# Optimization experiments

Measured on AMD Instinct MI355X. Metric: run time of the kernel, lower is better.

## Reference

```python
import jax, jax.numpy as jnp
import numpy as np

S, B, T, D = 256, 32, 24, 512


def setup_inputs() -> dict:
    key = jax.random.key(0)
    ks = jax.random.split(key, 30)
    def lin(k, out_d, in_d):
        kw, kb = jax.random.split(k)
        w = jax.random.normal(kw, (out_d, in_d), jnp.float32) * 0.02
        b = jax.random.normal(kb, (out_d,), jnp.float32) * 0.02
        return w, b
    inp = {
        'context_output': jax.random.normal(ks[0], (S, B, D), jnp.float32),
        'context_hidden_state': jax.random.normal(ks[1], (B, D), jnp.float32),
        'question_output': jax.random.normal(ks[2], (T, B, D), jnp.float32),
        'question_hidden_state': jax.random.normal(ks[3], (B, D), jnp.float32),
        'image_output': jax.random.normal(ks[4], (S, B, D), jnp.float32),
        'image_hidden_state': jax.random.normal(ks[5], (B, D), jnp.float32),
    }
    inp['fc1_w'], inp['fc1_b'] = lin(ks[6], D, D)
    inp['fc2_w'], inp['fc2_b'] = lin(ks[7], D, D)
    inp['dm_w'], inp['dm_b'] = lin(ks[8], D, D)
    inp['ms_w'], inp['ms_b'] = lin(ks[9], 1, D)
    inp['rm_w'], inp['rm_b'] = lin(ks[10], D, D)
    inp['qm_w'], inp['qm_b'] = lin(ks[11], D, D)
    inp['rr_w'], inp['rr_b'] = lin(ks[12], D, D)
    inp['rg_w'], inp['rg_b'] = lin(ks[13], D, D)
    inp['qg_w'], inp['qg_b'] = lin(ks[14], D, D)
    return inp


def reference(context_output, context_hidden_state, question_output,
              question_hidden_state, image_output, image_hidden_state,
              fc1_w, fc1_b, fc2_w, fc2_b, dm_w, dm_b, ms_w, ms_b,
              rm_w, rm_b, qm_w, qm_b, rr_w, rr_b, rg_w, rg_b, qg_w, qg_b):
    # context_output/image_output: [S,B,D] -> co: [B,S,D]
    co = (jnp.einsum('sbd,ed->bse', context_output, fc1_w) + fc1_b
          + jnp.einsum('sbd,ed->bse', image_output, fc2_w) + fc2_b)
    # linear_dm(co) is loop-invariant; compute once (same math as original)
    co_dm = jnp.einsum('bsd,ed->bse', co, dm_w) + dm_b  # [B,S,D]

    def step(r, q):
        # r: [B,D] (the original's [B,1,D] memory), q: [B,D]
        add = (r @ rm_w.T + rm_b) + (q @ qm_w.T + qm_b)  # [B,D]
        m = jnp.tanh(co_dm + add[:, None, :])             # [B,S,D]
        logits = m @ ms_w.T + ms_b                        # [B,S,1]
        s = jax.nn.softmax(logits, axis=1)                # softmax over S
        r_new = jnp.sum(s * co, axis=1) + jnp.tanh(r @ rr_w.T + rr_b)
        return r_new, None

    r0 = jnp.zeros((B, D), co.dtype)
    r, _ = jax.lax.scan(step, r0, question_output)  # scan over T steps
    g = (r @ rg_w.T + rg_b) + (question_hidden_state @ qg_w.T + qg_b)
    return g
```

## Files before the change

### kernel.cpp

```cpp
#include <hip/hip_runtime.h>

#define S_DIM 256
#define B_DIM 32
#define T_DIM 24
#define D_DIM 512

typedef short short8 __attribute__((ext_vector_type(8)));
typedef unsigned short ushort8 __attribute__((ext_vector_type(8)));
typedef float float4v __attribute__((ext_vector_type(4)));
typedef unsigned long long u64;

#define ATOM_ST64(p, v) __hip_atomic_store((p), (v), __ATOMIC_RELAXED, __HIP_MEMORY_SCOPE_AGENT)
#define ATOM_LD64(p)    __hip_atomic_load((p), __ATOMIC_RELAXED, __HIP_MEMORY_SCOPE_AGENT)

__device__ __forceinline__ float bf2f(unsigned short u) {
  union { unsigned int i; float f; } v; v.i = ((unsigned int)u) << 16; return v.f;
}
__device__ __forceinline__ unsigned short f2bf(float f) {
  union { float f; unsigned int i; } v; v.f = f;
  unsigned int i = v.i;
  return (unsigned short)((i + 0x7fffu + ((i >> 16) & 1u)) >> 16);
}
__device__ __forceinline__ float tanh_fast(float x) {
  float p = __builtin_amdgcn_exp2f(x * 2.885390082f);
  return 1.f - 2.f * __builtin_amdgcn_rcpf(1.f + p);
}
__device__ __forceinline__ void gload_lds16(const void* g, void* l) {
  __builtin_amdgcn_global_load_lds(
      (const __attribute__((address_space(1))) void*)g,
      (__attribute__((address_space(3))) void*)l, 16, 0, 0);
}
__device__ __forceinline__ u64 pack_tag(unsigned tag, float v) {
  union { float f; unsigned u; } c; c.f = v;
  return ((u64)tag << 32) | (u64)c.u;
}
__device__ __forceinline__ float unpack_val(u64 v) {
  union { unsigned u; float f; } c; c.u = (unsigned)v; return c.f;
}
__device__ __forceinline__ float poll_val(const u64* p, unsigned tag) {
  u64 v = ATOM_LD64(p);
  while ((unsigned)(v >> 32) != tag) { __builtin_amdgcn_s_sleep(1); v = ATOM_LD64(p); }
  return unpack_val(v);
}

template<bool A_F32, bool W_F32, bool DUAL, bool PERMUTE>
__global__ __launch_bounds__(256)
void gemm_nt(const void* __restrict__ A1v, const void* __restrict__ A2v,
             const void* __restrict__ W1v, const void* __restrict__ W2v,
             const float* __restrict__ bias1,
             const float* __restrict__ bias2,
             unsigned short* __restrict__ out)
{
  __shared__ unsigned short At[128 * 32] __attribute__((aligned(16)));
  __shared__ unsigned short Bt[128 * 32] __attribute__((aligned(16)));

  const int tid  = threadIdx.x;
  const int wid  = tid >> 6;
  const int lane = tid & 63;
  const int bm = blockIdx.x, bn = blockIdx.y;
  const int wm = (wid & 1) * 64, wn = (wid >> 1) * 64;

  float4v acc[4][4];
#pragma unroll
  for (int i = 0; i < 4; ++i)
#pragma unroll
    for (int jj = 0; jj < 4; ++jj) acc[i][jj] = (float4v){0.f, 0.f, 0.f, 0.f};

  const int NK = DUAL ? 32 : 16;
  for (int it = 0; it < NK; ++it) {
    const int kk = it * 32;
    const void* Av = A1v;
    const void* Wv = W1v;
    int ks = kk;
    if (DUAL && kk >= 512) { Av = A2v; Wv = W2v; ks = kk - 512; }

    __syncthreads();
    if (A_F32) {
      const float* Af = (const float*)Av;
      const int r = tid >> 1, h = tid & 1;
      const float4v* p = (const float4v*)(Af + (size_t)(bm * 128 + r) * 512 + ks + h * 16);
      float4v x0 = p[0], x1 = p[1], x2 = p[2], x3 = p[3];
      ushort8 u0, u1;
#pragma unroll
      for (int i = 0; i < 4; ++i) {
        u0[i] = f2bf(x0[i]); u0[i + 4] = f2bf(x1[i]);
        u1[i] = f2bf(x2[i]); u1[i + 4] = f2bf(x3[i]);
      }
      *(ushort8*)&At[r * 32 + h * 16] = u0;
      *(ushort8*)&At[r * 32 + h * 16 + 8] = u1;
    } else {
      const unsigned short* Ab = (const unsigned short*)Av;
#pragma unroll
      for (int i = 0; i < 2; ++i)
        gload_lds16(Ab + (size_t)(bm * 128 + wid * 32 + i * 16 + (lane >> 2)) * 512 + ks + (lane & 3) * 8,
                    &At[(wid * 32 + i * 16) * 32]);
    }
    if (W_F32) {
      const float* Wf = (const float*)Wv;
      const int r = tid >> 1, h = tid & 1;
      const float4v* p = (const float4v*)(Wf + (size_t)(bn * 128 + r) * 512 + ks + h * 16);
      float4v x0 = p[0], x1 = p[1], x2 = p[2], x3 = p[3];
      ushort8 u0, u1;
#pragma unroll
      for (int i = 0; i < 4; ++i) {
        u0[i] = f2bf(x0[i]); u0[i + 4] = f2bf(x1[i]);
        u1[i] = f2bf(x2[i]); u1[i + 4] = f2bf(x3[i]);
      }
      *(ushort8*)&Bt[r * 32 + h * 16] = u0;
      *(ushort8*)&Bt[r * 32 + h * 16 + 8] = u1;
    } else {
      const unsigned short* Wb = (const unsigned short*)Wv;
#pragma unroll
      for (int i = 0; i < 2; ++i)
        gload_lds16(Wb + (size_t)(bn * 128 + wid * 32 + i * 16 + (lane >> 2)) * 512 + ks + (lane & 3) * 8,
                    &Bt[(wid * 32 + i * 16) * 32]);
    }
    __syncthreads();

    short8 fa[4], fb[4];
#pragma unroll
    for (int mi = 0; mi < 4; ++mi)
      fa[mi] = *(const short8*)&At[(wm + mi * 16 + (lane & 15)) * 32 + (lane >> 4) * 8];
#pragma unroll
    for (int ni = 0; ni < 4; ++ni)
      fb[ni] = *(const short8*)&Bt[(wn + ni * 16 + (lane & 15)) * 32 + (lane >> 4) * 8];
#pragma unroll
    for (int mi = 0; mi < 4; ++mi)
#pragma unroll
      for (int ni = 0; ni < 4; ++ni)
        acc[mi][ni] = __builtin_amdgcn_mfma_f32_16x16x32_bf16(fa[mi], fb[ni], acc[mi][ni], 0, 0, 0);
  }

#pragma unroll
  for (int mi = 0; mi < 4; ++mi) {
    const int row0 = wm + mi * 16 + (lane >> 4) * 4;
#pragma unroll
    for (int ni = 0; ni < 4; ++ni) {
      const int col = bn * 128 + wn + ni * 16 + (lane & 15);
      float bsum = 0.f;
      if (bias1) bsum += bias1[col];
      if (bias2) bsum += bias2[col];
#pragma unroll
      for (int i = 0; i < 4; ++i) {
        const int m = bm * 128 + row0 + i;
        const int orow = PERMUTE ? ((m & 31) * 256 + (m >> 5)) : m;
        out[(size_t)orow * 512 + col] = f2bf(acc[mi][ni][i] + bsum);
      }
    }
  }
}

__global__ __launch_bounds__(512)
void scan_kernel(const unsigned short* __restrict__ co,
                 const unsigned short* __restrict__ codm,
                 const float* __restrict__ qo,
                 u64* __restrict__ addT,
                 u64* __restrict__ rrtT,
                 u64* __restrict__ denT,
                 u64* __restrict__ pvecT,
                 const float* __restrict__ ms_w,
                 const float* __restrict__ rm_w,
                 const float* __restrict__ rr_w,
                 const float* __restrict__ rr_b,
                 const float* __restrict__ qm_w,
                 const float* __restrict__ qm_b,
                 const float* __restrict__ rm_b,
                 const float* __restrict__ qhs,
                 const float* __restrict__ rg_w,
                 const float* __restrict__ qg_w,
                 const float* __restrict__ rg_b,
                 const float* __restrict__ qg_b,
                 float* __restrict__ outg)
{
  __shared__ unsigned short scrS[32 * 520] __attribute__((aligned(16)));
  __shared__ float rS[512];
  __shared__ float addS[512] __attribute__((aligned(16)));
  __shared__ float msS[512] __attribute__((aligned(16)));
  __shared__ float partS[512];
  __shared__ float partR[512];
  __shared__ float wS[32];
  __shared__ float rrbS[64];
  __shared__ float qmrmS[64];
  __shared__ float denS[8];
  __shared__ float qaddS[T_DIM * 64];

  const int tid  = threadIdx.x;
  const int wid  = tid >> 6;
  const int lane = tid & 63;
  const int b = blockIdx.x >> 3;
  const int j = blockIdx.x & 7;

  ushort8 rmp[8], rrp[8], qmp[8];
  for (int pass = 0; pass < 6; ++pass) {
    const float* Wsrc = (pass < 2) ? rm_w : (pass < 4) ? rr_w : qm_w;
    const int rbase = (pass & 1) * 32;
    for (int r = wid; r < 32; r += 8) {
      const float* src = &Wsrc[(size_t)(j * 64 + rbase + r) * 512 + lane * 8];
      float4v a = *(const float4v*)src;
      float4v c = *(const float4v*)(src + 4);
      ushort8 u8;
#pragma unroll
      for (int i = 0; i < 4; ++i) { u8[i] = f2bf(a[i]); u8[i + 4] = f2bf(c[i]); }
      *(ushort8*)&scrS[r * 520 + lane * 8] = u8;
    }
    __syncthreads();
    if ((lane >> 5) == (pass & 1)) {
      const int rloc = lane & 31;
#pragma unroll
      for (int u = 0; u < 8; ++u) {
        ushort8 v = *(const ushort8*)&scrS[rloc * 520 + wid * 64 + u * 8];
        if (pass < 2) rmp[u] = v; else if (pass < 4) rrp[u] = v; else qmp[u] = v;
      }
    }
    __syncthreads();
  }

  msS[tid] = ms_w[tid];
  if (tid < 64) {
    rrbS[tid]  = rr_b[j * 64 + tid];
    qmrmS[tid] = qm_b[j * 64 + tid] + rm_b[j * 64 + tid];
  }
  rS[tid] = 0.f;

  float* qoS = (float*)scrS;
  for (int half = 0; half < 2; ++half) {
    __syncthreads();
#pragma unroll
    for (int i = 0; i < 3; ++i) {
      const int f4 = tid + i * 512;
      const int tl = f4 >> 7, c4 = f4 & 127;
      ((float4v*)qoS)[f4] =
          *(const float4v*)&qo[((size_t)(half * 12 + tl) * 32 + b) * 512 + c4 * 4];
    }
    __syncthreads();
    for (int tl = 0; tl < 12; ++tl) {
      float p = 0.f;
#pragma unroll
      for (int u = 0; u < 8; ++u) {
        ushort8 w8 = qmp[u];
#pragma unroll
        for (int i2 = 0; i2 < 8; ++i2)
          p = fmaf(qoS[tl * 512 + wid * 64 + u * 8 + i2], bf2f(w8[i2]), p);
      }
      partS[wid * 64 + lane] = p;
      __syncthreads();
      if (wid == 0) {
        float s = 0.f;
#pragma unroll
        for (int w2 = 0; w2 < 8; ++w2) s += partS[w2 * 64 + lane];
        qaddS[(half * 12 + tl) * 64 + lane] = s + qmrmS[lane];
      }
      __syncthreads();
    }
  }

  const size_t gbase = ((size_t)b * 256 + j * 32) * 512;
  for (int idx = tid; idx < 2048; idx += 512)
    *(ushort8*)&scrS[idx * 8] = *(const ushort8*)&codm[gbase + (size_t)idx * 8];
  const unsigned short* cdS = scrS;
  __syncthreads();

  for (int t = 0; t < T_DIM; ++t) {
    const unsigned tagA = 2u * (unsigned)t + 1u;
    const unsigned tagB = 2u * (unsigned)t + 2u;

    float am = 0.f, ar = 0.f;
#pragma unroll
    for (int u = 0; u < 8; ++u) {
      ushort8 wm8 = rmp[u], wr8 = rrp[u];
#pragma unroll
      for (int i2 = 0; i2 < 8; ++i2) {
        const float rv = rS[wid * 64 + u * 8 + i2];
        am = fmaf(rv, bf2f(wm8[i2]), am);
        ar = fmaf(rv, bf2f(wr8[i2]), ar);
      }
    }
    partS[wid * 64 + lane] = am;
    partR[wid * 64 + lane] = ar;
    __syncthreads();
    if (wid == 0) {
      float s = 0.f;
#pragma unroll
      for (int w2 = 0; w2 < 8; ++w2) s += partS[w2 * 64 + lane];
      s += qaddS[t * 64 + lane];
      ATOM_ST64(&addT[b * 512 + j * 64 + lane], pack_tag(tagA, s));
    } else if (wid == 1) {
      float s = 0.f;
#pragma unroll
      for (int w2 = 0; w2 < 8; ++w2) s += partR[w2 * 64 + lane];
      ATOM_ST64(&rrtT[(size_t)(t & 1) * (B_DIM * 512) + b * 512 + j * 64 + lane],
                pack_tag(tagA, tanh_fast(s + rrbS[lane])));
    }
    addS[tid] = poll_val(&addT[b * 512 + tid], tagA);
    __syncthreads();

#pragma unroll
    for (int q = 0; q < 4; ++q) {
      const int sl = wid * 4 + q;
      ushort8 cd8 = *(const ushort8*)&cdS[sl * 512 + lane * 8];
      float4v a0 = *(const float4v*)&addS[lane * 8];
      float4v a1 = *(const float4v*)&addS[lane * 8 + 4];
      float4v m0 = *(const float4v*)&msS[lane * 8];
      float4v m1 = *(const float4v*)&msS[lane * 8 + 4];
      float acc = 0.f;
#pragma unroll
      for (int i = 0; i < 4; ++i) {
        acc = fmaf(tanh_fast(bf2f(cd8[i]) + a0[i]), m0[i], acc);
        acc = fmaf(tanh_fast(bf2f(cd8[i + 4]) + a1[i]), m1[i], acc);
      }
#pragma unroll
      for (int off = 32; off > 0; off >>= 1) acc += __shfl_xor(acc, off, 64);
      if (lane == 0) wS[sl] = __builtin_amdgcn_exp2f(acc * 1.44269504f);
    }
    __syncthreads();

    {
      float accv = 0.f;
#pragma unroll 8
      for (int sl = 0; sl < 32; ++sl)
        accv = fmaf(wS[sl], bf2f(co[gbase + (size_t)sl * 512 + tid]), accv);
      ATOM_ST64(&pvecT[((size_t)b * 8 + j) * 512 + tid], pack_tag(tagB, accv));
      if (tid == 0) {
        float dsum = 0.f;
        for (int sl = 0; sl < 32; ++sl) dsum += wS[sl];
        ATOM_ST64(&denT[b * 8 + j], pack_tag(tagB, dsum));
      }
    }

    u64 pv[8];
#pragma unroll
    for (int jj = 0; jj < 8; ++jj)
      pv[jj] = ATOM_LD64(&pvecT[((size_t)b * 8 + jj) * 512 + tid]);
    u64 rv64 = ATOM_LD64(&rrtT[(size_t)(t & 1) * (B_DIM * 512) + b * 512 + tid]);
    if (tid < 8) denS[tid] = poll_val(&denT[b * 8 + tid], tagB);
    float sum = 0.f;
#pragma unroll
    for (int jj = 0; jj < 8; ++jj) {
      while ((unsigned)(pv[jj] >> 32) != tagB) {
        __builtin_amdgcn_s_sleep(1);
        pv[jj] = ATOM_LD64(&pvecT[((size_t)b * 8 + jj) * 512 + tid]);
      }
      sum += unpack_val(pv[jj]);
    }
    while ((unsigned)(rv64 >> 32) != tagA) {
      __builtin_amdgcn_s_sleep(1);
      rv64 = ATOM_LD64(&rrtT[(size_t)(t & 1) * (B_DIM * 512) + b * 512 + tid]);
    }
    __syncthreads();
    const float den = denS[0] + denS[1] + denS[2] + denS[3] +
                      denS[4] + denS[5] + denS[6] + denS[7];
    rS[tid] = sum * __builtin_amdgcn_rcpf(den) + unpack_val(rv64);
    __syncthreads();
  }

  addS[tid] = qhs[b * 512 + tid];
  __syncthreads();
  {
    const int e = j * 64 + lane;
    const float* rgp = rg_w + (size_t)e * 512 + wid * 64;
    const float* qgp = qg_w + (size_t)e * 512 + wid * 64;
    float acc = 0.f;
#pragma unroll
    for (int u = 0; u < 8; ++u) {
      float4v g0 = *(const float4v*)&rgp[u * 8];
      float4v g1 = *(const float4v*)&rgp[u * 8 + 4];
      float4v q0 = *(const float4v*)&qgp[u * 8];
      float4v q1 = *(const float4v*)&qgp[u * 8 + 4];
#pragma unroll
      for (int i2 = 0; i2 < 4; ++i2) {
        acc = fmaf(rS[wid * 64 + u * 8 + i2],     g0[i2], acc);
        acc = fmaf(rS[wid * 64 + u * 8 + 4 + i2], g1[i2], acc);
        acc = fmaf(addS[wid * 64 + u * 8 + i2],     q0[i2], acc);
        acc = fmaf(addS[wid * 64 + u * 8 + 4 + i2], q1[i2], acc);
      }
    }
    partS[wid * 64 + lane] = acc;
  }
  __syncthreads();
  if (wid == 0) {
    float s = 0.f;
#pragma unroll
    for (int w2 = 0; w2 < 8; ++w2) s += partS[w2 * 64 + lane];
    const int e = j * 64 + lane;
    s += rg_b[e] + qg_b[e];
    outg[b * 512 + e] = s;
  }
}

extern "C" void kernel_launch(void* const* d_in, const int* in_sizes, int n_in,
                              void* d_out, int out_size, void* d_ws, size_t ws_size,
                              hipStream_t stream)
{
  (void)in_sizes; (void)n_in; (void)out_size; (void)ws_size;
  const float* ctx  = (const float*)d_in[0];
  const float* qo   = (const float*)d_in[2];
  const float* qhs  = (const float*)d_in[3];
  const float* img  = (const float*)d_in[4];
  const float* fc1w = (const float*)d_in[6];
  const float* fc1b = (const float*)d_in[7];
  const float* fc2w = (const float*)d_in[8];
  const float* fc2b = (const float*)d_in[9];
  const float* dmw  = (const float*)d_in[10];
  const float* dmb  = (const float*)d_in[11];
  const float* msw  = (const float*)d_in[12];
  const float* rmw  = (const float*)d_in[14];
  const float* rmb  = (const float*)d_in[15];
  const float* qmw  = (const float*)d_in[16];
  const float* qmb  = (const float*)d_in[17];
  const float* rrw  = (const float*)d_in[18];
  const float* rrb  = (const float*)d_in[19];
  const float* rgw  = (const float*)d_in[20];
  const float* rgb  = (const float*)d_in[21];
  const float* qgw  = (const float*)d_in[22];
  const float* qgb  = (const float*)d_in[23];

  char* ws = (char*)d_ws;
  u64* addT  = (u64*)ws;
  u64* rrtT  = addT + B_DIM * 512;
  u64* denT  = rrtT + 2 * B_DIM * 512;
  u64* pvecT = denT + B_DIM * 8;
  unsigned short* co   = (unsigned short*)(pvecT + (size_t)B_DIM * 8 * 512);
  unsigned short* codm = co + (size_t)B_DIM * S_DIM * D_DIM;
  const size_t tagBytes = (size_t)(131072 + 262144 + 2048 + 1048576);

  hipMemsetAsync(ws, 0, tagBytes, stream);
  gemm_nt<true, true, true, true><<<dim3(64, 4), 256, 0, stream>>>(
      ctx, img, fc1w, fc2w, fc1b, fc2b, co);
  gemm_nt<false, true, false, false><<<dim3(64, 4), 256, 0, stream>>>(
      co, nullptr, dmw, nullptr, dmb, nullptr, codm);
  scan_kernel<<<256, 512, 0, stream>>>(co, codm, qo, addT, rrtT, denT, pvecT,
                                       msw, rmw, rrw, rrb, qmw, qmb, rmb, qhs,
                                       rgw, qgw, rgb, qgb, (float*)d_out);
}
```

Baseline: 420.6 us.

## Pre-convert GEMM inputs to bf16, shrink GEMM N-tile, and restructure scan step sync

```diff
diff --git a/kernel.cpp b/kernel.cpp
--- a/kernel.cpp
+++ b/kernel.cpp
@@ -7,6 +7,7 @@
 
 typedef short short8 __attribute__((ext_vector_type(8)));
 typedef unsigned short ushort8 __attribute__((ext_vector_type(8)));
+typedef unsigned short ushort4v __attribute__((ext_vector_type(4)));
 typedef float float4v __attribute__((ext_vector_type(4)));
 typedef unsigned long long u64;
 
@@ -43,91 +44,85 @@
   return unpack_val(v);
 }
 
-template<bool A_F32, bool W_F32, bool DUAL, bool PERMUTE>
 __global__ __launch_bounds__(256)
-void gemm_nt(const void* __restrict__ A1v, const void* __restrict__ A2v,
-             const void* __restrict__ W1v, const void* __restrict__ W2v,
+void cvt_kernel(const float* __restrict__ s0, const float* __restrict__ s1,
+                const float* __restrict__ s2, const float* __restrict__ s3,
+                const float* __restrict__ s4,
+                unsigned short* __restrict__ d0, unsigned short* __restrict__ d1,
+                unsigned short* __restrict__ d2, unsigned short* __restrict__ d3,
+                unsigned short* __restrict__ d4)
+{
+  const int idx = blockIdx.x * 256 + threadIdx.x;
+  const float* s; unsigned short* d; int off;
+  if (idx < 2097152) {
+    off = idx & 1048575;
+    if (idx < 1048576) { s = s0; d = d0; } else { s = s1; d = d1; }
+  } else {
+    const int k = (idx - 2097152) >> 16;
+    off = (idx - 2097152) & 65535;
+    if (k == 0)      { s = s2; d = d2; }
+    else if (k == 1) { s = s3; d = d3; }
+    else             { s = s4; d = d4; }
+  }
+  const float4v v = ((const float4v*)s)[off];
+  ushort4v u;
+  u[0] = f2bf(v[0]); u[1] = f2bf(v[1]); u[2] = f2bf(v[2]); u[3] = f2bf(v[3]);
+  ((ushort4v*)d)[off] = u;
+}
+
+template<bool DUAL, bool PERMUTE>
+__global__ __launch_bounds__(256)
+void gemm_nt(const unsigned short* __restrict__ A1,
+             const unsigned short* __restrict__ A2,
+             const unsigned short* __restrict__ W1,
+             const unsigned short* __restrict__ W2,
              const float* __restrict__ bias1,
              const float* __restrict__ bias2,
              unsigned short* __restrict__ out)
 {
   __shared__ unsigned short At[128 * 32] __attribute__((aligned(16)));
-  __shared__ unsigned short Bt[128 * 32] __attribute__((aligned(16)));
+  __shared__ unsigned short Bt[64 * 32] __attribute__((aligned(16)));
 
   const int tid  = threadIdx.x;
   const int wid  = tid >> 6;
   const int lane = tid & 63;
   const int bm = blockIdx.x, bn = blockIdx.y;
-  const int wm = (wid & 1) * 64, wn = (wid >> 1) * 64;
-
-  float4v acc[4][4];
+  const int wm = (wid & 1) * 64, wn = (wid >> 1) * 32;
+
+  float4v acc[4][2];
 #pragma unroll
   for (int i = 0; i < 4; ++i)
 #pragma unroll
-    for (int jj = 0; jj < 4; ++jj) acc[i][jj] = (float4v){0.f, 0.f, 0.f, 0.f};
+    for (int jj = 0; jj < 2; ++jj) acc[i][jj] = (float4v){0.f, 0.f, 0.f, 0.f};
 
   const int NK = DUAL ? 32 : 16;
   for (int it = 0; it < NK; ++it) {
     const int kk = it * 32;
-    const void* Av = A1v;
-    const void* Wv = W1v;
+    const unsigned short* As = A1;
+    const unsigned short* Ws = W1;
     int ks = kk;
-    if (DUAL && kk >= 512) { Av = A2v; Wv = W2v; ks = kk - 512; }
-
-    __syncthreads();
-    if (A_F32) {
-      const float* Af = (const float*)Av;
-      const int r = tid >> 1, h = tid & 1;
-      const float4v* p = (const float4v*)(Af + (size_t)(bm * 128 + r) * 512 + ks + h * 16);
-      float4v x0 = p[0], x1 = p[1], x2 = p[2], x3 = p[3];
-      ushort8 u0, u1;
-#pragma unroll
-      for (int i = 0; i < 4; ++i) {
-        u0[i] = f2bf(x0[i]); u0[i + 4] = f2bf(x1[i]);
-        u1[i] = f2bf(x2[i]); u1[i + 4] = f2bf(x3[i]);
-      }
-      *(ushort8*)&At[r * 32 + h * 16] = u0;
-      *(ushort8*)&At[r * 32 + h * 16 + 8] = u1;
-    } else {
-      const unsigned short* Ab = (const unsigned short*)Av;
-#pragma unroll
-      for (int i = 0; i < 2; ++i)
-        gload_lds16(Ab + (size_t)(bm * 128 + wid * 32 + i * 16 + (lane >> 2)) * 512 + ks + (lane & 3) * 8,
-                    &At[(wid * 32 + i * 16) * 32]);
-    }
-    if (W_F32) {
-      const float* Wf = (const float*)Wv;
-      const int r = tid >> 1, h = tid & 1;
-      const float4v* p = (const float4v*)(Wf + (size_t)(bn * 128 + r) * 512 + ks + h * 16);
-      float4v x0 = p[0], x1 = p[1], x2 = p[2], x3 = p[3];
-      ushort8 u0, u1;
-#pragma unroll
-      for (int i = 0; i < 4; ++i) {
-        u0[i] = f2bf(x0[i]); u0[i + 4] = f2bf(x1[i]);
-        u1[i] = f2bf(x2[i]); u1[i + 4] = f2bf(x3[i]);
-      }
-      *(ushort8*)&Bt[r * 32 + h * 16] = u0;
-      *(ushort8*)&Bt[r * 32 + h * 16 + 8] = u1;
-    } else {
-      const unsigned short* Wb = (const unsigned short*)Wv;
-#pragma unroll
-      for (int i = 0; i < 2; ++i)
-        gload_lds16(Wb + (size_t)(bn * 128 + wid * 32 + i * 16 + (lane >> 2)) * 512 + ks + (lane & 3) * 8,
-                    &Bt[(wid * 32 + i * 16) * 32]);
-    }
-    __syncthreads();
-
-    short8 fa[4], fb[4];
+    if (DUAL && kk >= 512) { As = A2; Ws = W2; ks = kk - 512; }
+
+    __syncthreads();
+#pragma unroll
+    for (int i = 0; i < 2; ++i)
+      gload_lds16(As + (size_t)(bm * 128 + wid * 32 + i * 16 + (lane >> 2)) * 512 + ks + (lane & 3) * 8,
+                  &At[(wid * 32 + i * 16) * 32]);
+    gload_lds16(Ws + (size_t)(bn * 64 + wid * 16 + (lane >> 2)) * 512 + ks + (lane & 3) * 8,
+                &Bt[(wid * 16) * 32]);
+    __syncthreads();
+
+    short8 fa[4], fb[2];
 #pragma unroll
     for (int mi = 0; mi < 4; ++mi)
       fa[mi] = *(const short8*)&At[(wm + mi * 16 + (lane & 15)) * 32 + (lane >> 4) * 8];
 #pragma unroll
-    for (int ni = 0; ni < 4; ++ni)
+    for (int ni = 0; ni < 2; ++ni)
       fb[ni] = *(const short8*)&Bt[(wn + ni * 16 + (lane & 15)) * 32 + (lane >> 4) * 8];
 #pragma unroll
     for (int mi = 0; mi < 4; ++mi)
 #pragma unroll
-      for (int ni = 0; ni < 4; ++ni)
+      for (int ni = 0; ni < 2; ++ni)
         acc[mi][ni] = __builtin_amdgcn_mfma_f32_16x16x32_bf16(fa[mi], fb[ni], acc[mi][ni], 0, 0, 0);
   }
 
@@ -135,8 +130,8 @@
   for (int mi = 0; mi < 4; ++mi) {
     const int row0 = wm + mi * 16 + (lane >> 4) * 4;
 #pragma unroll
-    for (int ni = 0; ni < 4; ++ni) {
-      const int col = bn * 128 + wn + ni * 16 + (lane & 15);
+    for (int ni = 0; ni < 2; ++ni) {
+      const int col = bn * 64 + wn + ni * 16 + (lane & 15);
       float bsum = 0.f;
       if (bias1) bsum += bias1[col];
       if (bias2) bsum += bias2[col];
@@ -174,15 +169,18 @@
 {
   __shared__ unsigned short scrS[32 * 520] __attribute__((aligned(16)));
   __shared__ float rS[512];
-  __shared__ float addS[512] __attribute__((aligned(16)));
-  __shared__ float msS[512] __attribute__((aligned(16)));
+  __shared__ float addS[512];
+  __shared__ float msS[512];
   __shared__ float partS[512];
   __shared__ float partR[512];
+  __shared__ float rrtS[512];
+  __shared__ float pvS[512];
   __shared__ float wS[32];
   __shared__ float rrbS[64];
   __shared__ float qmrmS[64];
   __shared__ float denS[8];
   __shared__ float qaddS[T_DIM * 64];
+  __shared__ int flagS[8];
 
   const int tid  = threadIdx.x;
   const int wid  = tid >> 6;
@@ -220,7 +218,7 @@
     rrbS[tid]  = rr_b[j * 64 + tid];
     qmrmS[tid] = qm_b[j * 64 + tid] + rm_b[j * 64 + tid];
   }
-  rS[tid] = 0.f;
+  if (tid < 8) flagS[tid] = 0;
 
   float* qoS = (float*)scrS;
   for (int half = 0; half < 2; ++half) {
@@ -242,48 +240,41 @@
         for (int i2 = 0; i2 < 8; ++i2)
           p = fmaf(qoS[tl * 512 + wid * 64 + u * 8 + i2], bf2f(w8[i2]), p);
       }
-      partS[wid * 64 + lane] = p;
+      float* pbuf = (tl & 1) ? partR : partS;
+      pbuf[wid * 64 + lane] = p;
       __syncthreads();
-      if (wid == 0) {
+      if (wid == (tl & 1)) {
         float s = 0.f;
 #pragma unroll
-        for (int w2 = 0; w2 < 8; ++w2) s += partS[w2 * 64 + lane];
+        for (int w2 = 0; w2 < 8; ++w2) s += pbuf[w2 * 64 + lane];
         qaddS[(half * 12 + tl) * 64 + lane] = s + qmrmS[lane];
       }
-      __syncthreads();
-    }
+    }
+    __syncthreads();
   }
 
   const size_t gbase = ((size_t)b * 256 + j * 32) * 512;
   for (int idx = tid; idx < 2048; idx += 512)
     *(ushort8*)&scrS[idx * 8] = *(const ushort8*)&codm[gbase + (size_t)idx * 8];
   const unsigned short* cdS = scrS;
-  __syncthreads();
+
+  partS[tid] = 0.f;
+  partR[tid] = 0.f;
 
   for (int t = 0; t < T_DIM; ++t) {
     const unsigned tagA = 2u * (unsigned)t + 1u;
     const unsigned tagB = 2u * (unsigned)t + 2u;
-
-    float am = 0.f, ar = 0.f;
-#pragma unroll
-    for (int u = 0; u < 8; ++u) {
-      ushort8 wm8 = rmp[u], wr8 = rrp[u];
-#pragma unroll
-      for (int i2 = 0; i2 < 8; ++i2) {
-        const float rv = rS[wid * 64 + u * 8 + i2];
-        am = fmaf(rv, bf2f(wm8[i2]), am);
-        ar = fmaf(rv, bf2f(wr8[i2]), ar);
-      }
-    }
-    partS[wid * 64 + lane] = am;
-    partR[wid * 64 + lane] = ar;
-    __syncthreads();
+    __syncthreads();
+
     if (wid == 0) {
       float s = 0.f;
 #pragma unroll
       for (int w2 = 0; w2 < 8; ++w2) s += partS[w2 * 64 + lane];
       s += qaddS[t * 64 + lane];
       ATOM_ST64(&addT[b * 512 + j * 64 + lane], pack_tag(tagA, s));
+      addS[j * 64 + lane] = s;
+      __threadfence_block();
+      if (lane == 0) ((volatile int*)flagS)[j] = t + 1;
     } else if (wid == 1) {
       float s = 0.f;
 #pragma unroll
@@ -291,26 +282,34 @@
       ATOM_ST64(&rrtT[(size_t)(t & 1) * (B_DIM * 512) + b * 512 + j * 64 + lane],
                 pack_tag(tagA, tanh_fast(s + rrbS[lane])));
     }
-    addS[tid] = poll_val(&addT[b * 512 + tid], tagA);
-    __syncthreads();
-
+    if (wid != j) {
+      float v = poll_val(&addT[b * 512 + wid * 64 + lane], tagA);
+      addS[wid * 64 + lane] = v;
+      __threadfence_block();
+      if (lane == 0) ((volatile int*)flagS)[wid] = t + 1;
+    }
+
+    float aq0 = 0.f, aq1 = 0.f, aq2 = 0.f, aq3 = 0.f;
+    const int sl0 = wid * 4;
+#pragma unroll
+    for (int i = 0; i < 8; ++i) {
+      const int jj = (j + i) & 7;
+      while (((volatile int*)flagS)[jj] != t + 1) {}
+      __threadfence_block();
+      const int e = jj * 64 + lane;
+      const float av = addS[e];
+      const float mv = msS[e];
+      aq0 = fmaf(mv, tanh_fast(bf2f(cdS[(sl0 + 0) * 512 + e]) + av), aq0);
+      aq1 = fmaf(mv, tanh_fast(bf2f(cdS[(sl0 + 1) * 512 + e]) + av), aq1);
+      aq2 = fmaf(mv, tanh_fast(bf2f(cdS[(sl0 + 2) * 512 + e]) + av), aq2);
+      aq3 = fmaf(mv, tanh_fast(bf2f(cdS[(sl0 + 3) * 512 + e]) + av), aq3);
+    }
+    float aq[4] = {aq0, aq1, aq2, aq3};
 #pragma unroll
     for (int q = 0; q < 4; ++q) {
-      const int sl = wid * 4 + q;
-      ushort8 cd8 = *(const ushort8*)&cdS[sl * 512 + lane * 8];
-      float4v a0 = *(const float4v*)&addS[lane * 8];
-      float4v a1 = *(const float4v*)&addS[lane * 8 + 4];
-      float4v m0 = *(const float4v*)&msS[lane * 8];
-      float4v m1 = *(const float4v*)&msS[lane * 8 + 4];
-      float acc = 0.f;
-#pragma unroll
-      for (int i = 0; i < 4; ++i) {
-        acc = fmaf(tanh_fast(bf2f(cd8[i]) + a0[i]), m0[i], acc);
-        acc = fmaf(tanh_fast(bf2f(cd8[i + 4]) + a1[i]), m1[i], acc);
-      }
-#pragma unroll
-      for (int off = 32; off > 0; off >>= 1) acc += __shfl_xor(acc, off, 64);
-      if (lane == 0) wS[sl] = __builtin_amdgcn_exp2f(acc * 1.44269504f);
+#pragma unroll
+      for (int off = 32; off > 0; off >>= 1) aq[q] += __shfl_xor(aq[q], off, 64);
+      if (lane == 0) wS[sl0 + q] = __builtin_amdgcn_exp2f(aq[q] * 1.44269504f);
     }
     __syncthreads();
 
@@ -320,11 +319,12 @@
       for (int sl = 0; sl < 32; ++sl)
         accv = fmaf(wS[sl], bf2f(co[gbase + (size_t)sl * 512 + tid]), accv);
       ATOM_ST64(&pvecT[((size_t)b * 8 + j) * 512 + tid], pack_tag(tagB, accv));
-      if (tid == 0) {
-        float dsum = 0.f;
-        for (int sl = 0; sl < 32; ++sl) dsum += wS[sl];
-        ATOM_ST64(&denT[b * 8 + j], pack_tag(tagB, dsum));
-      }
+    }
+    if (wid == 0) {
+      float dv = (lane < 32) ? wS[lane] : 0.f;
+#pragma unroll
+      for (int off = 32; off > 0; off >>= 1) dv += __shfl_xor(dv, off, 64);
+      if (lane == 0) ATOM_ST64(&denT[b * 8 + j], pack_tag(tagB, dv));
     }
 
     u64 pv[8];
@@ -332,7 +332,25 @@
     for (int jj = 0; jj < 8; ++jj)
       pv[jj] = ATOM_LD64(&pvecT[((size_t)b * 8 + jj) * 512 + tid]);
     u64 rv64 = ATOM_LD64(&rrtT[(size_t)(t & 1) * (B_DIM * 512) + b * 512 + tid]);
-    if (tid < 8) denS[tid] = poll_val(&denT[b * 8 + tid], tagB);
+    if (wid == 0 && lane < 8) denS[lane] = poll_val(&denT[b * 8 + lane], tagB);
+    while ((unsigned)(rv64 >> 32) != tagA) {
+      __builtin_amdgcn_s_sleep(1);
+      rv64 = ATOM_LD64(&rrtT[(size_t)(t & 1) * (B_DIM * 512) + b * 512 + tid]);
+    }
+    rrtS[tid] = unpack_val(rv64);
+    __syncthreads();
+
+    float am = 0.f, ar = 0.f;
+#pragma unroll
+    for (int u = 0; u < 8; ++u) {
+      ushort8 wm8 = rmp[u], wr8 = rrp[u];
+#pragma unroll
+      for (int i2 = 0; i2 < 8; ++i2) {
+        const float rv = rrtS[wid * 64 + u * 8 + i2];
+        am = fmaf(rv, bf2f(wm8[i2]), am);
+        ar = fmaf(rv, bf2f(wr8[i2]), ar);
+      }
+    }
     float sum = 0.f;
 #pragma unroll
     for (int jj = 0; jj < 8; ++jj) {
@@ -342,17 +360,28 @@
       }
       sum += unpack_val(pv[jj]);
     }
-    while ((unsigned)(rv64 >> 32) != tagA) {
-      __builtin_amdgcn_s_sleep(1);
-      rv64 = ATOM_LD64(&rrtT[(size_t)(t & 1) * (B_DIM * 512) + b * 512 + tid]);
-    }
-    __syncthreads();
     const float den = denS[0] + denS[1] + denS[2] + denS[3] +
                       denS[4] + denS[5] + denS[6] + denS[7];
-    rS[tid] = sum * __builtin_amdgcn_rcpf(den) + unpack_val(rv64);
-    __syncthreads();
-  }
-
+    const float pvs = sum * __builtin_amdgcn_rcpf(den);
+    pvS[tid] = pvs;
+    rS[tid]  = pvs + rrtS[tid];
+    __syncthreads();
+
+#pragma unroll
+    for (int u = 0; u < 8; ++u) {
+      ushort8 wm8 = rmp[u], wr8 = rrp[u];
+#pragma unroll
+      for (int i2 = 0; i2 < 8; ++i2) {
+        const float pvv = pvS[wid * 64 + u * 8 + i2];
+        am = fmaf(pvv, bf2f(wm8[i2]), am);
+        ar = fmaf(pvv, bf2f(wr8[i2]), ar);
+      }
+    }
+    partS[wid * 64 + lane] = am;
+    partR[wid * 64 + lane] = ar;
+  }
+
+  __syncthreads();
   addS[tid] = qhs[b * 512 + tid];
   __syncthreads();
   {
@@ -419,15 +448,22 @@
   u64* rrtT  = addT + B_DIM * 512;
   u64* denT  = rrtT + 2 * B_DIM * 512;
   u64* pvecT = denT + B_DIM * 8;
-  unsigned short* co   = (unsigned short*)(pvecT + (size_t)B_DIM * 8 * 512);
-  unsigned short* codm = co + (size_t)B_DIM * S_DIM * D_DIM;
+  unsigned short* co    = (unsigned short*)(pvecT + (size_t)B_DIM * 8 * 512);
+  unsigned short* codm  = co + (size_t)B_DIM * S_DIM * D_DIM;
+  unsigned short* ctxb  = codm + (size_t)B_DIM * S_DIM * D_DIM;
+  unsigned short* imgb  = ctxb + (size_t)S_DIM * B_DIM * D_DIM;
+  unsigned short* fc1wb = imgb + (size_t)S_DIM * B_DIM * D_DIM;
+  unsigned short* fc2wb = fc1wb + D_DIM * D_DIM;
+  unsigned short* dmwb  = fc2wb + D_DIM * D_DIM;
   const size_t tagBytes = (size_t)(131072 + 262144 + 2048 + 1048576);
 
   hipMemsetAsync(ws, 0, tagBytes, stream);
-  gemm_nt<true, true, true, true><<<dim3(64, 4), 256, 0, stream>>>(
-      ctx, img, fc1w, fc2w, fc1b, fc2b, co);
-  gemm_nt<false, true, false, false><<<dim3(64, 4), 256, 0, stream>>>(
-      co, nullptr, dmw, nullptr, dmb, nullptr, codm);
+  cvt_kernel<<<8960, 256, 0, stream>>>(ctx, img, fc1w, fc2w, dmw,
+                                       ctxb, imgb, fc1wb, fc2wb, dmwb);
+  gemm_nt<true, true><<<dim3(64, 8), 256, 0, stream>>>(
+      ctxb, imgb, fc1wb, fc2wb, fc1b, fc2b, co);
+  gemm_nt<false, false><<<dim3(64, 8), 256, 0, stream>>>(
+      co, nullptr, dmwb, nullptr, dmb, nullptr, codm);
   scan_kernel<<<256, 512, 0, stream>>>(co, codm, qo, addT, rrtT, denT, pvecT,
                                        msw, rmw, rrw, rrb, qmw, qmb, rmb, qhs,
                                        rgw, qgw, rgb, qgb, (float*)d_out);
```

After: 522.0 us. 24.1% more time.
